# Performance work log

Hardware: AMD Instinct MI355X
Metric: run time of the kernel (lower is better)

Reference implementation:

```python
import jax, jax.numpy as jnp
import numpy as np

N, D_IN, D_BLOCK, D_OUT, E, K = 65536, 128, 256, 128, 8, 2


def setup_inputs() -> dict:
    key = jax.random.key(0)
    ks = jax.random.split(key, 8)
    s_in = 1.0 / np.sqrt(D_IN)
    s_h = 1.0 / np.sqrt(D_BLOCK)
    return {
        "x": jax.random.normal(ks[0], (N, D_IN), jnp.float32),
        "Wg": jax.random.normal(ks[1], (D_IN, E), jnp.float32) * s_in,
        "W1": jax.random.normal(ks[2], (E, D_IN, D_BLOCK), jnp.float32) * s_in,
        "b1": jax.random.normal(ks[3], (E, D_BLOCK), jnp.float32) * 0.01,
        "W2": jax.random.normal(ks[4], (E, D_BLOCK, D_BLOCK), jnp.float32) * s_h,
        "b2": jax.random.normal(ks[5], (E, D_BLOCK), jnp.float32) * 0.01,
        "Wo": jax.random.normal(ks[6], (D_BLOCK, D_OUT), jnp.float32) * s_h,
        "bo": jax.random.normal(ks[7], (D_OUT,), jnp.float32) * 0.01,
    }


def reference(x, Wg, W1, b1, W2, b2, Wo, bo):
    # Router: linear gate -> top-k -> softmax over the k selected logits,
    # scattered back to a dense [N, E] combine-weight matrix (zeros elsewhere).
    logits = x @ Wg                                   # [N, E]
    topv, topi = jax.lax.top_k(logits, K)             # [N, K]
    w_topk = jax.nn.softmax(topv, axis=-1)            # [N, K]
    onehot = jax.nn.one_hot(topi, E, dtype=x.dtype)   # [N, K, E]
    weights = jnp.einsum("nk,nke->ne", w_topk, onehot)  # [N, E]

    # Expert MLPs (n_blocks=2, ReLU, dropout=0 at eval), computed for all
    # experts over all tokens; unselected experts have weight 0, so the
    # weighted combine reproduces the original masked gather/scatter math.
    h = jax.nn.relu(jnp.einsum("nd,edh->enh", x, W1) + b1[:, None, :])   # [E,N,H]
    h = jax.nn.relu(jnp.einsum("enh,ehg->eng", h, W2) + b2[:, None, :])  # [E,N,H]
    y = jnp.einsum("enh,ho->eno", h, Wo) + bo                             # [E,N,O]

    # Weighted scatter-add combine: outs[n] = sum_e weights[n,e] * y[e,n]
    return jnp.einsum("ne,eno->no", weights, y)
```

## Files before the change

kernel.cpp:

```cpp
#include <hip/hip_runtime.h>
#include <math.h>

typedef unsigned short ushort_t;
typedef __attribute__((ext_vector_type(8))) short bf16x8;
typedef __attribute__((ext_vector_type(4))) float f32x4;
typedef __attribute__((ext_vector_type(8))) unsigned short u16x8;

#define N_TOK 65536
#define DIN 128
#define HD 256
#define DOUT 128
#define NEXP 8
#define MT 64
#define MAX_TILES (N_TOK / MT)

__device__ __forceinline__ unsigned short f2bf(float f) {
    union { float f; unsigned int i; } v; v.f = f;
    unsigned int i = v.i;
    return (unsigned short)((i + 0x7FFFu + ((i >> 16) & 1u)) >> 16);
}

__global__ void pack_weights(const float* __restrict__ W1,
                             const float* __restrict__ W2,
                             const float* __restrict__ Wo,
                             ushort_t* __restrict__ wt1f,
                             ushort_t* __restrict__ wt2f,
                             ushort_t* __restrict__ wotf) {
    int id = blockIdx.x * 256 + threadIdx.x;
    const float* src; ushort_t* dst; int Nn, ksteps, c;
    if (id < 32768) {
        int e = id >> 12; c = id & 4095;
        Nn = HD; ksteps = 4; src = W1 + (size_t)e * DIN * HD; dst = wt1f + (size_t)id * 8;
    } else if (id < 98304) {
        int t = id - 32768; int e = t >> 13; c = t & 8191;
        Nn = HD; ksteps = 8; src = W2 + (size_t)e * HD * HD; dst = wt2f + (size_t)t * 8;
    } else {
        int t = id - 98304; c = t;
        Nn = DOUT; ksteps = 8; src = Wo; dst = wotf + (size_t)t * 8;
    }
    int L = c & 63; int kc = c >> 6;
    int kstep = kc % ksteps; int ntile = kc / ksteps;
    int q = L >> 4, m = L & 15;
    int n = ntile * 16 + m; int k0 = kstep * 32 + q * 8;
    u16x8 v;
#pragma unroll
    for (int j = 0; j < 8; j++) v[j] = f2bf(src[(size_t)(k0 + j) * Nn + n]);
    *(u16x8*)dst = v;
}

#define RT_BLOCK 512
#define RT_TPB 64
__global__ __launch_bounds__(RT_BLOCK)
void router_kernel(const float* __restrict__ x,
                   const float* __restrict__ Wg,
                   int* __restrict__ counts,
                   int* __restrict__ list_tok,
                   float* __restrict__ list_w) {
    __shared__ float wgsT[NEXP * 132];
    __shared__ int lcnt[NEXP];
    __shared__ int lbase[NEXP];
    int tid = threadIdx.x;
    if (tid < NEXP) lcnt[tid] = 0;
    for (int i = tid; i < DIN * NEXP; i += RT_BLOCK) {
        int e = i & 7, k = i >> 3;
        wgsT[e * 132 + k] = Wg[i];
    }
    __syncthreads();

    int e = tid & 7;
    int tl = tid >> 3;
    int n = blockIdx.x * RT_TPB + tl;
    const float4* xr = (const float4*)(x + (size_t)n * DIN);
    const float4* wv4 = (const float4*)(wgsT + e * 132);
    float lg = 0.f;
#pragma unroll
    for (int kk = 0; kk < 32; kk++) {
        float4 xv = xr[kk];
        float4 wv = wv4[kk];
        lg += xv.x * wv.x;
        lg += xv.y * wv.y;
        lg += xv.z * wv.z;
        lg += xv.w * wv.w;
    }
    float v0 = lg; int e0 = e;
#pragma unroll
    for (int d = 1; d < 8; d <<= 1) {
        float ov = __shfl_xor(v0, d, 64);
        int oe = __shfl_xor(e0, d, 64);
        if (ov > v0 || (ov == v0 && oe < e0)) { v0 = ov; e0 = oe; }
    }
    float mv = (e == e0) ? -3.0e38f : lg;
    float v1 = mv; int e1 = e;
#pragma unroll
    for (int d = 1; d < 8; d <<= 1) {
        float ov = __shfl_xor(v1, d, 64);
        int oe = __shfl_xor(e1, d, 64);
        if (ov > v1 || (ov == v1 && oe < e1)) { v1 = ov; e1 = oe; }
    }
    float t = expf(v1 - v0);
    float inv = 1.0f / (1.0f + t);
    float w0 = inv, w1 = t * inv;

    bool writer = (e == 0);
    int p0 = 0, p1 = 0;
    if (writer) {
        p0 = atomicAdd(&lcnt[e0], 1);
        p1 = atomicAdd(&lcnt[e1], 1);
    }
    __syncthreads();
    if (tid < NEXP) lbase[tid] = atomicAdd(&counts[tid], lcnt[tid]);
    __syncthreads();
    if (writer) {
        int q0 = lbase[e0] + p0;
        list_tok[e0 * N_TOK + q0] = n;
        list_w[e0 * N_TOK + q0] = w0;
        int q1 = lbase[e1] + p1;
        list_tok[e1 * N_TOK + q1] = n;
        list_w[e1 * N_TOK + q1] = w1;
    }
}

__global__ void init_out(const float* __restrict__ bo, float* __restrict__ out) {
    int gid = blockIdx.x * 256 + threadIdx.x;
    float4 b = ((const float4*)bo)[gid & 31];
    ((float4*)out)[gid] = b;
}

__global__ __launch_bounds__(256, 3)
void expert_kernel(const float* __restrict__ x,
                   const int* __restrict__ counts,
                   const int* __restrict__ list_tok,
                   const float* __restrict__ list_w,
                   const ushort_t* __restrict__ wt1f,
                   const ushort_t* __restrict__ wt2f,
                   const ushort_t* __restrict__ wotf,
                   const float* __restrict__ b1,
                   const float* __restrict__ b2,
                   float* __restrict__ out) {
    int e = blockIdx.x & 7;
    int tile = blockIdx.x >> 3;
    int cnt = counts[e];
    int base = tile * MT;
    if (base >= cnt) return;
    int rows = cnt - base; if (rows > MT) rows = MT;

    __shared__ __align__(16) ushort_t bufA[8192];
    __shared__ __align__(16) ushort_t bufH[16384];
    __shared__ int toks_s[MT];
    __shared__ float wts_s[MT];

    int tid = threadIdx.x;
    int lane = tid & 63;
    int w = tid >> 6;
    int q = lane >> 4;
    int mcol = lane & 15;

    if (tid < MT) {
        int rr = tid < rows ? tid : rows - 1;
        toks_s[tid] = list_tok[(size_t)e * N_TOK + base + rr];
        wts_s[tid] = list_w[(size_t)e * N_TOK + base + rr];
    }
    for (int c = tid; c < 1024; c += 256) {
        int row = c >> 4;
        int kchunk = c & 15;
        int rr = row < rows ? row : rows - 1;
        int tok = list_tok[(size_t)e * N_TOK + base + rr];
        const float4* src = (const float4*)(x + (size_t)tok * DIN + kchunk * 8);
        float4 lo = src[0], hi = src[1];
        u16x8 v;
        v[0] = f2bf(lo.x); v[1] = f2bf(lo.y); v[2] = f2bf(lo.z); v[3] = f2bf(lo.w);
        v[4] = f2bf(hi.x); v[5] = f2bf(hi.y); v[6] = f2bf(hi.z); v[7] = f2bf(hi.w);
        int kstep = kchunk >> 2, qq = kchunk & 3;
        int dchunk = (kstep * 4 + (row >> 4)) * 64 + qq * 16 + (row & 15);
        ((u16x8*)bufA)[dchunk] = v;
    }
    __syncthreads();

    const bf16x8* Albs = (const bf16x8*)bufA;
    const bf16x8* Hlbs = (const bf16x8*)bufH;

    f32x4 acc[4][4];
#pragma unroll
    for (int mt = 0; mt < 4; mt++)
#pragma unroll
        for (int nt = 0; nt < 4; nt++) acc[mt][nt] = (f32x4){0.f, 0.f, 0.f, 0.f};
    const bf16x8* B1 = (const bf16x8*)(wt1f + (size_t)e * 4096 * 8);
#pragma unroll
    for (int kstep = 0; kstep < 4; kstep++) {
        bf16x8 a[4];
#pragma unroll
        for (int mt = 0; mt < 4; mt++) a[mt] = Albs[(kstep * 4 + mt) * 64 + lane];
#pragma unroll
        for (int nt = 0; nt < 4; nt++) {
            bf16x8 b = B1[((w * 4 + nt) * 4 + kstep) * 64 + lane];
#pragma unroll
            for (int mt = 0; mt < 4; mt++)
                acc[mt][nt] = __builtin_amdgcn_mfma_f32_16x16x32_bf16(a[mt], b, acc[mt][nt], 0, 0, 0);
        }
    }
#pragma unroll
    for (int nt = 0; nt < 4; nt++) {
        int nn = (w * 4 + nt) * 16 + mcol;
        float bias = b1[e * HD + nn];
        int kstep = nn >> 5, qq = (nn >> 3) & 3, jj = nn & 7;
#pragma unroll
        for (int mt = 0; mt < 4; mt++) {
#pragma unroll
            for (int r = 0; r < 4; r++) {
                float v = acc[mt][nt][r] + bias;
                v = v > 0.f ? v : 0.f;
                int chunk = (kstep * 4 + mt) * 64 + qq * 16 + q * 4 + r;
                bufH[chunk * 8 + jj] = f2bf(v);
            }
        }
    }
    __syncthreads();

    f32x4 acc2[4][4];
#pragma unroll
    for (int mt = 0; mt < 4; mt++)
#pragma unroll
        for (int nt = 0; nt < 4; nt++) acc2[mt][nt] = (f32x4){0.f, 0.f, 0.f, 0.f};
    const bf16x8* B2 = (const bf16x8*)(wt2f + (size_t)e * 8192 * 8);
#pragma unroll
    for (int kstep = 0; kstep < 8; kstep++) {
        bf16x8 a[4];
#pragma unroll
        for (int mt = 0; mt < 4; mt++) a[mt] = Hlbs[(kstep * 4 + mt) * 64 + lane];
#pragma unroll
        for (int nt = 0; nt < 4; nt++) {
            bf16x8 b = B2[((w * 4 + nt) * 8 + kstep) * 64 + lane];
#pragma unroll
            for (int mt = 0; mt < 4; mt++)
                acc2[mt][nt] = __builtin_amdgcn_mfma_f32_16x16x32_bf16(a[mt], b, acc2[mt][nt], 0, 0, 0);
        }
    }
    __syncthreads();
#pragma unroll
    for (int nt = 0; nt < 4; nt++) {
        int nn = (w * 4 + nt) * 16 + mcol;
        float bias = b2[e * HD + nn];
        int kstep = nn >> 5, qq = (nn >> 3) & 3, jj = nn & 7;
#pragma unroll
        for (int mt = 0; mt < 4; mt++) {
#pragma unroll
            for (int r = 0; r < 4; r++) {
                float v = acc2[mt][nt][r] + bias;
                v = v > 0.f ? v : 0.f;
                int chunk = (kstep * 4 + mt) * 64 + qq * 16 + q * 4 + r;
                bufH[chunk * 8 + jj] = f2bf(v);
            }
        }
    }
    __syncthreads();

    f32x4 acc3[4][2];
#pragma unroll
    for (int mt = 0; mt < 4; mt++)
#pragma unroll
        for (int nt = 0; nt < 2; nt++) acc3[mt][nt] = (f32x4){0.f, 0.f, 0.f, 0.f};
    const bf16x8* B3 = (const bf16x8*)wotf;
#pragma unroll
    for (int kstep = 0; kstep < 8; kstep++) {
        bf16x8 a[4];
#pragma unroll
        for (int mt = 0; mt < 4; mt++) a[mt] = Hlbs[(kstep * 4 + mt) * 64 + lane];
#pragma unroll
        for (int nt = 0; nt < 2; nt++) {
            bf16x8 b = B3[((w * 2 + nt) * 8 + kstep) * 64 + lane];
#pragma unroll
            for (int mt = 0; mt < 4; mt++)
                acc3[mt][nt] = __builtin_amdgcn_mfma_f32_16x16x32_bf16(a[mt], b, acc3[mt][nt], 0, 0, 0);
        }
    }
#pragma unroll
    for (int mt = 0; mt < 4; mt++) {
#pragma unroll
        for (int r = 0; r < 4; r++) {
            int row = mt * 16 + q * 4 + r;
            if (row < rows) {
                int tok = toks_s[row];
                float wgt = wts_s[row];
                float* dst = out + (size_t)tok * DOUT;
#pragma unroll
                for (int nt = 0; nt < 2; nt++) {
                    int col = (w * 2 + nt) * 16 + mcol;
                    atomicAdd(&dst[col], wgt * acc3[mt][nt][r]);
                }
            }
        }
    }
}

extern "C" void kernel_launch(void* const* d_in, const int* in_sizes, int n_in,
                              void* d_out, int out_size, void* d_ws, size_t ws_size,
                              hipStream_t stream) {
    const float* x  = (const float*)d_in[0];
    const float* Wg = (const float*)d_in[1];
    const float* W1 = (const float*)d_in[2];
    const float* b1 = (const float*)d_in[3];
    const float* W2 = (const float*)d_in[4];
    const float* b2 = (const float*)d_in[5];
    const float* Wo = (const float*)d_in[6];
    const float* bo = (const float*)d_in[7];
    float* out = (float*)d_out;

    char* ws = (char*)d_ws;
    size_t off = 0;
    int* counts    = (int*)(ws + off);    off += 256;
    int* list_tok  = (int*)(ws + off);    off += (size_t)NEXP * N_TOK * 4;
    float* list_w  = (float*)(ws + off);  off += (size_t)NEXP * N_TOK * 4;
    ushort_t* wt1f = (ushort_t*)(ws + off); off += (size_t)NEXP * DIN * HD * 2;
    ushort_t* wt2f = (ushort_t*)(ws + off); off += (size_t)NEXP * HD * HD * 2;
    ushort_t* wotf = (ushort_t*)(ws + off); off += (size_t)HD * DOUT * 2;

    hipMemsetAsync(counts, 0, 256, stream);
    pack_weights<<<400, 256, 0, stream>>>(W1, W2, Wo, wt1f, wt2f, wotf);
    router_kernel<<<N_TOK / RT_TPB, RT_BLOCK, 0, stream>>>(x, Wg, counts, list_tok, list_w);
    init_out<<<(N_TOK * DOUT / 4) / 256, 256, 0, stream>>>(bo, out);
    expert_kernel<<<NEXP * MAX_TILES, 256, 0, stream>>>(x, counts, list_tok, list_w,
                                                        wt1f, wt2f, wotf, b1, b2, out);
}
```

Baseline: 199.8 us.

## Fuse packing and output init into router, prefetch weights, use transposed LDS reads

Folds the weight-packing and output-bias initialization kernels into the router kernel, removing two launches. In the expert kernel, weight fragments are double-buffered in registers to prefetch the next k-step, biases are hoisted, and f32->bf16 conversion uses packed v_cvt_pk_bf16_f32. Hidden activations are now stored row-major with vectorized 8-byte writes and read back with ds_read_b64_tr_b16 transposed LDS loads instead of scalar 2-byte scattered stores. This raises register pressure and relies on inline asm with manual waitcnt.

Result: faster. 178.8 us (-10.5%).

```diff
diff --git a/kernel.cpp b/kernel.cpp
--- a/kernel.cpp
+++ b/kernel.cpp
@@ -3,8 +3,11 @@
 
 typedef unsigned short ushort_t;
 typedef __attribute__((ext_vector_type(8))) short bf16x8;
+typedef __attribute__((ext_vector_type(4))) short bf16x4;
 typedef __attribute__((ext_vector_type(4))) float f32x4;
 typedef __attribute__((ext_vector_type(8))) unsigned short u16x8;
+typedef __attribute__((ext_vector_type(2))) unsigned int u32x2;
+typedef __attribute__((ext_vector_type(4))) unsigned int u32x4;
 
 #define N_TOK 65536
 #define DIN 128
@@ -20,50 +23,62 @@
     return (unsigned short)((i + 0x7FFFu + ((i >> 16) & 1u)) >> 16);
 }
 
-__global__ void pack_weights(const float* __restrict__ W1,
-                             const float* __restrict__ W2,
-                             const float* __restrict__ Wo,
-                             ushort_t* __restrict__ wt1f,
-                             ushort_t* __restrict__ wt2f,
-                             ushort_t* __restrict__ wotf) {
-    int id = blockIdx.x * 256 + threadIdx.x;
-    const float* src; ushort_t* dst; int Nn, ksteps, c;
-    if (id < 32768) {
-        int e = id >> 12; c = id & 4095;
-        Nn = HD; ksteps = 4; src = W1 + (size_t)e * DIN * HD; dst = wt1f + (size_t)id * 8;
-    } else if (id < 98304) {
-        int t = id - 32768; int e = t >> 13; c = t & 8191;
-        Nn = HD; ksteps = 8; src = W2 + (size_t)e * HD * HD; dst = wt2f + (size_t)t * 8;
-    } else {
-        int t = id - 98304; c = t;
-        Nn = DOUT; ksteps = 8; src = Wo; dst = wotf + (size_t)t * 8;
-    }
-    int L = c & 63; int kc = c >> 6;
-    int kstep = kc % ksteps; int ntile = kc / ksteps;
-    int q = L >> 4, m = L & 15;
-    int n = ntile * 16 + m; int k0 = kstep * 32 + q * 8;
-    u16x8 v;
-#pragma unroll
-    for (int j = 0; j < 8; j++) v[j] = f2bf(src[(size_t)(k0 + j) * Nn + n]);
-    *(u16x8*)dst = v;
-}
-
 #define RT_BLOCK 512
 #define RT_TPB 64
+
 __global__ __launch_bounds__(RT_BLOCK)
 void router_kernel(const float* __restrict__ x,
                    const float* __restrict__ Wg,
+                   const float* __restrict__ W1,
+                   const float* __restrict__ W2,
+                   const float* __restrict__ Wo,
+                   const float* __restrict__ bo,
                    int* __restrict__ counts,
                    int* __restrict__ list_tok,
-                   float* __restrict__ list_w) {
+                   float* __restrict__ list_w,
+                   ushort_t* __restrict__ wt1f,
+                   ushort_t* __restrict__ wt2f,
+                   ushort_t* __restrict__ wotf,
+                   float* __restrict__ out) {
     __shared__ float wgsT[NEXP * 132];
     __shared__ int lcnt[NEXP];
     __shared__ int lbase[NEXP];
     int tid = threadIdx.x;
     if (tid < NEXP) lcnt[tid] = 0;
     for (int i = tid; i < DIN * NEXP; i += RT_BLOCK) {
-        int e = i & 7, k = i >> 3;
-        wgsT[e * 132 + k] = Wg[i];
+        int ee = i & 7, k = i >> 3;
+        wgsT[ee * 132 + k] = Wg[i];
+    }
+    {
+        const float4* bo4 = (const float4*)bo;
+        float4* ob = (float4*)(out + (size_t)blockIdx.x * RT_TPB * DOUT);
+#pragma unroll
+        for (int i = 0; i < 4; i++) {
+            int idx = i * RT_BLOCK + tid;
+            ob[idx] = bo4[idx & 31];
+        }
+    }
+    if (blockIdx.x < 200) {
+        int id = blockIdx.x * RT_BLOCK + tid;
+        const float* src; ushort_t* dst; int Nn, ksteps, c;
+        if (id < 32768) {
+            int ee = id >> 12; c = id & 4095;
+            Nn = HD; ksteps = 4; src = W1 + (size_t)ee * DIN * HD; dst = wt1f + (size_t)id * 8;
+        } else if (id < 98304) {
+            int t = id - 32768; int ee = t >> 13; c = t & 8191;
+            Nn = HD; ksteps = 8; src = W2 + (size_t)ee * HD * HD; dst = wt2f + (size_t)t * 8;
+        } else {
+            int t = id - 98304; c = t;
+            Nn = DOUT; ksteps = 8; src = Wo; dst = wotf + (size_t)t * 8;
+        }
+        int L = c & 63; int kc = c >> 6;
+        int kstep = kc % ksteps; int ntile = kc / ksteps;
+        int qq = L >> 4, mm = L & 15;
+        int n = ntile * 16 + mm; int k0 = kstep * 32 + qq * 8;
+        u16x8 v;
+#pragma unroll
+        for (int j = 0; j < 8; j++) v[j] = f2bf(src[(size_t)(k0 + j) * Nn + n]);
+        *(u16x8*)dst = v;
     }
     __syncthreads();
 
@@ -118,12 +133,6 @@
         list_tok[e1 * N_TOK + q1] = n;
         list_w[e1 * N_TOK + q1] = w1;
     }
-}
-
-__global__ void init_out(const float* __restrict__ bo, float* __restrict__ out) {
-    int gid = blockIdx.x * 256 + threadIdx.x;
-    float4 b = ((const float4*)bo)[gid & 31];
-    ((float4*)out)[gid] = b;
 }
 
 __global__ __launch_bounds__(256, 3)
@@ -160,6 +169,19 @@
         toks_s[tid] = list_tok[(size_t)e * N_TOK + base + rr];
         wts_s[tid] = list_w[(size_t)e * N_TOK + base + rr];
     }
+
+    float bias1[4], bias2[4];
+#pragma unroll
+    for (int nt = 0; nt < 4; nt++) {
+        int nn = (w * 4 + nt) * 16 + mcol;
+        bias1[nt] = b1[e * HD + nn];
+        bias2[nt] = b2[e * HD + nn];
+    }
+    const bf16x8* B1 = (const bf16x8*)(wt1f + (size_t)e * 4096 * 8);
+    bf16x8 b1r[2][4];
+#pragma unroll
+    for (int nt = 0; nt < 4; nt++) b1r[0][nt] = B1[((w * 4 + nt) * 4 + 0) * 64 + lane];
+
     for (int c = tid; c < 1024; c += 256) {
         int row = c >> 4;
         int kchunk = c & 15;
@@ -167,89 +189,120 @@
         int tok = list_tok[(size_t)e * N_TOK + base + rr];
         const float4* src = (const float4*)(x + (size_t)tok * DIN + kchunk * 8);
         float4 lo = src[0], hi = src[1];
-        u16x8 v;
-        v[0] = f2bf(lo.x); v[1] = f2bf(lo.y); v[2] = f2bf(lo.z); v[3] = f2bf(lo.w);
-        v[4] = f2bf(hi.x); v[5] = f2bf(hi.y); v[6] = f2bf(hi.z); v[7] = f2bf(hi.w);
+        unsigned p0, p1, p2, p3;
+        asm("v_cvt_pk_bf16_f32 %0, %1, %2" : "=v"(p0) : "v"(lo.x), "v"(lo.y));
+        asm("v_cvt_pk_bf16_f32 %0, %1, %2" : "=v"(p1) : "v"(lo.z), "v"(lo.w));
+        asm("v_cvt_pk_bf16_f32 %0, %1, %2" : "=v"(p2) : "v"(hi.x), "v"(hi.y));
+        asm("v_cvt_pk_bf16_f32 %0, %1, %2" : "=v"(p3) : "v"(hi.z), "v"(hi.w));
         int kstep = kchunk >> 2, qq = kchunk & 3;
         int dchunk = (kstep * 4 + (row >> 4)) * 64 + qq * 16 + (row & 15);
-        ((u16x8*)bufA)[dchunk] = v;
+        u32x4 v; v.x = p0; v.y = p1; v.z = p2; v.w = p3;
+        *(u32x4*)(&bufA[dchunk * 8]) = v;
     }
     __syncthreads();
 
     const bf16x8* Albs = (const bf16x8*)bufA;
-    const bf16x8* Hlbs = (const bf16x8*)bufH;
 
     f32x4 acc[4][4];
 #pragma unroll
     for (int mt = 0; mt < 4; mt++)
 #pragma unroll
         for (int nt = 0; nt < 4; nt++) acc[mt][nt] = (f32x4){0.f, 0.f, 0.f, 0.f};
-    const bf16x8* B1 = (const bf16x8*)(wt1f + (size_t)e * 4096 * 8);
 #pragma unroll
     for (int kstep = 0; kstep < 4; kstep++) {
+        const int cur = kstep & 1, nxt = cur ^ 1;
+        if (kstep < 3) {
+#pragma unroll
+            for (int nt = 0; nt < 4; nt++)
+                b1r[nxt][nt] = B1[((w * 4 + nt) * 4 + kstep + 1) * 64 + lane];
+        }
         bf16x8 a[4];
 #pragma unroll
         for (int mt = 0; mt < 4; mt++) a[mt] = Albs[(kstep * 4 + mt) * 64 + lane];
 #pragma unroll
-        for (int nt = 0; nt < 4; nt++) {
-            bf16x8 b = B1[((w * 4 + nt) * 4 + kstep) * 64 + lane];
+        for (int nt = 0; nt < 4; nt++)
 #pragma unroll
             for (int mt = 0; mt < 4; mt++)
-                acc[mt][nt] = __builtin_amdgcn_mfma_f32_16x16x32_bf16(a[mt], b, acc[mt][nt], 0, 0, 0);
-        }
-    }
+                acc[mt][nt] = __builtin_amdgcn_mfma_f32_16x16x32_bf16(a[mt], b1r[cur][nt], acc[mt][nt], 0, 0, 0);
+    }
+
+    const bf16x8* B2 = (const bf16x8*)(wt2f + (size_t)e * 8192 * 8);
+    bf16x8 b2r[2][4];
+#pragma unroll
+    for (int nt = 0; nt < 4; nt++) b2r[0][nt] = B2[((w * 4 + nt) * 8 + 0) * 64 + lane];
+
 #pragma unroll
     for (int nt = 0; nt < 4; nt++) {
-        int nn = (w * 4 + nt) * 16 + mcol;
-        float bias = b1[e * HD + nn];
-        int kstep = nn >> 5, qq = (nn >> 3) & 3, jj = nn & 7;
+        int off0 = w * 2048 + nt * 512 + (mcol >> 2) * 128 + (mcol & 3) * 32 + q * 8;
 #pragma unroll
         for (int mt = 0; mt < 4; mt++) {
-#pragma unroll
-            for (int r = 0; r < 4; r++) {
-                float v = acc[mt][nt][r] + bias;
-                v = v > 0.f ? v : 0.f;
-                int chunk = (kstep * 4 + mt) * 64 + qq * 16 + q * 4 + r;
-                bufH[chunk * 8 + jj] = f2bf(v);
-            }
-        }
-    }
-    __syncthreads();
+            float v0 = acc[mt][nt][0] + bias1[nt]; v0 = v0 > 0.f ? v0 : 0.f;
+            float v1 = acc[mt][nt][1] + bias1[nt]; v1 = v1 > 0.f ? v1 : 0.f;
+            float v2 = acc[mt][nt][2] + bias1[nt]; v2 = v2 > 0.f ? v2 : 0.f;
+            float v3 = acc[mt][nt][3] + bias1[nt]; v3 = v3 > 0.f ? v3 : 0.f;
+            unsigned d0, d1;
+            asm("v_cvt_pk_bf16_f32 %0, %1, %2" : "=v"(d0) : "v"(v0), "v"(v1));
+            asm("v_cvt_pk_bf16_f32 %0, %1, %2" : "=v"(d1) : "v"(v2), "v"(v3));
+            u32x2 dd; dd.x = d0; dd.y = d1;
+            *(u32x2*)(&bufH[(mt * 8192 + off0) >> 1]) = dd;
+        }
+    }
+    __syncthreads();
+
+    unsigned trb = ((unsigned)(size_t)(void*)bufH) + (unsigned)(q * 256 + mcol * 8);
 
     f32x4 acc2[4][4];
 #pragma unroll
     for (int mt = 0; mt < 4; mt++)
 #pragma unroll
         for (int nt = 0; nt < 4; nt++) acc2[mt][nt] = (f32x4){0.f, 0.f, 0.f, 0.f};
-    const bf16x8* B2 = (const bf16x8*)(wt2f + (size_t)e * 8192 * 8);
 #pragma unroll
     for (int kstep = 0; kstep < 8; kstep++) {
+        const int cur = kstep & 1, nxt = cur ^ 1;
+        if (kstep < 7) {
+#pragma unroll
+            for (int nt = 0; nt < 4; nt++)
+                b2r[nxt][nt] = B2[((w * 4 + nt) * 8 + kstep + 1) * 64 + lane];
+        }
         bf16x8 a[4];
 #pragma unroll
-        for (int mt = 0; mt < 4; mt++) a[mt] = Hlbs[(kstep * 4 + mt) * 64 + lane];
-#pragma unroll
-        for (int nt = 0; nt < 4; nt++) {
-            bf16x8 b = B2[((w * 4 + nt) * 8 + kstep) * 64 + lane];
+        for (int mt = 0; mt < 4; mt++) {
+            bf16x4 lo, hi;
+            unsigned ad = trb + (unsigned)(mt * 8192 + kstep * 1024);
+            asm volatile("ds_read_b64_tr_b16 %0, %2\n\t"
+                         "ds_read_b64_tr_b16 %1, %2 offset:128"
+                         : "=&v"(lo), "=&v"(hi) : "v"(ad));
+            a[mt] = __builtin_shufflevector(lo, hi, 0, 1, 2, 3, 4, 5, 6, 7);
+        }
+        asm volatile("s_waitcnt lgkmcnt(0)" ::: "memory");
+        __builtin_amdgcn_sched_barrier(0);
+#pragma unroll
+        for (int nt = 0; nt < 4; nt++)
 #pragma unroll
             for (int mt = 0; mt < 4; mt++)
-                acc2[mt][nt] = __builtin_amdgcn_mfma_f32_16x16x32_bf16(a[mt], b, acc2[mt][nt], 0, 0, 0);
-        }
-    }
-    __syncthreads();
+                acc2[mt][nt] = __builtin_amdgcn_mfma_f32_16x16x32_bf16(a[mt], b2r[cur][nt], acc2[mt][nt], 0, 0, 0);
+    }
+    __syncthreads();
+
+    const bf16x8* B3 = (const bf16x8*)wotf;
+    bf16x8 b3r[2][2];
+#pragma unroll
+    for (int nt = 0; nt < 2; nt++) b3r[0][nt] = B3[((w * 2 + nt) * 8 + 0) * 64 + lane];
+
 #pragma unroll
     for (int nt = 0; nt < 4; nt++) {
-        int nn = (w * 4 + nt) * 16 + mcol;
-        float bias = b2[e * HD + nn];
-        int kstep = nn >> 5, qq = (nn >> 3) & 3, jj = nn & 7;
+        int off0 = w * 2048 + nt * 512 + (mcol >> 2) * 128 + (mcol & 3) * 32 + q * 8;
 #pragma unroll
         for (int mt = 0; mt < 4; mt++) {
-#pragma unroll
-            for (int r = 0; r < 4; r++) {
-                float v = acc2[mt][nt][r] + bias;
-                v = v > 0.f ? v : 0.f;
-                int chunk = (kstep * 4 + mt) * 64 + qq * 16 + q * 4 + r;
-                bufH[chunk * 8 + jj] = f2bf(v);
-            }
+            float v0 = acc2[mt][nt][0] + bias2[nt]; v0 = v0 > 0.f ? v0 : 0.f;
+            float v1 = acc2[mt][nt][1] + bias2[nt]; v1 = v1 > 0.f ? v1 : 0.f;
+            float v2 = acc2[mt][nt][2] + bias2[nt]; v2 = v2 > 0.f ? v2 : 0.f;
+            float v3 = acc2[mt][nt][3] + bias2[nt]; v3 = v3 > 0.f ? v3 : 0.f;
+            unsigned d0, d1;
+            asm("v_cvt_pk_bf16_f32 %0, %1, %2" : "=v"(d0) : "v"(v0), "v"(v1));
+            asm("v_cvt_pk_bf16_f32 %0, %1, %2" : "=v"(d1) : "v"(v2), "v"(v3));
+            u32x2 dd; dd.x = d0; dd.y = d1;
+            *(u32x2*)(&bufH[(mt * 8192 + off0) >> 1]) = dd;
         }
     }
     __syncthreads();
@@ -259,19 +312,31 @@
     for (int mt = 0; mt < 4; mt++)
 #pragma unroll
         for (int nt = 0; nt < 2; nt++) acc3[mt][nt] = (f32x4){0.f, 0.f, 0.f, 0.f};
-    const bf16x8* B3 = (const bf16x8*)wotf;
 #pragma unroll
     for (int kstep = 0; kstep < 8; kstep++) {
+        const int cur = kstep & 1, nxt = cur ^ 1;
+        if (kstep < 7) {
+#pragma unroll
+            for (int nt = 0; nt < 2; nt++)
+                b3r[nxt][nt] = B3[((w * 2 + nt) * 8 + kstep + 1) * 64 + lane];
+        }
         bf16x8 a[4];
 #pragma unroll
-        for (int mt = 0; mt < 4; mt++) a[mt] = Hlbs[(kstep * 4 + mt) * 64 + lane];
-#pragma unroll
-        for (int nt = 0; nt < 2; nt++) {
-            bf16x8 b = B3[((w * 2 + nt) * 8 + kstep) * 64 + lane];
+        for (int mt = 0; mt < 4; mt++) {
+            bf16x4 lo, hi;
+            unsigned ad = trb + (unsigned)(mt * 8192 + kstep * 1024);
+            asm volatile("ds_read_b64_tr_b16 %0, %2\n\t"
+                         "ds_read_b64_tr_b16 %1, %2 offset:128"
+                         : "=&v"(lo), "=&v"(hi) : "v"(ad));
+            a[mt] = __builtin_shufflevector(lo, hi, 0, 1, 2, 3, 4, 5, 6, 7);
+        }
+        asm volatile("s_waitcnt lgkmcnt(0)" ::: "memory");
+        __builtin_amdgcn_sched_barrier(0);
+#pragma unroll
+        for (int nt = 0; nt < 2; nt++)
 #pragma unroll
             for (int mt = 0; mt < 4; mt++)
-                acc3[mt][nt] = __builtin_amdgcn_mfma_f32_16x16x32_bf16(a[mt], b, acc3[mt][nt], 0, 0, 0);
-        }
+                acc3[mt][nt] = __builtin_amdgcn_mfma_f32_16x16x32_bf16(a[mt], b3r[cur][nt], acc3[mt][nt], 0, 0, 0);
     }
 #pragma unroll
     for (int mt = 0; mt < 4; mt++) {
@@ -315,9 +380,8 @@
     ushort_t* wotf = (ushort_t*)(ws + off); off += (size_t)HD * DOUT * 2;
 
     hipMemsetAsync(counts, 0, 256, stream);
-    pack_weights<<<400, 256, 0, stream>>>(W1, W2, Wo, wt1f, wt2f, wotf);
-    router_kernel<<<N_TOK / RT_TPB, RT_BLOCK, 0, stream>>>(x, Wg, counts, list_tok, list_w);
-    init_out<<<(N_TOK * DOUT / 4) / 256, 256, 0, stream>>>(bo, out);
+    router_kernel<<<N_TOK / RT_TPB, RT_BLOCK, 0, stream>>>(
+        x, Wg, W1, W2, Wo, bo, counts, list_tok, list_w, wt1f, wt2f, wotf, out);
     expert_kernel<<<NEXP * MAX_TILES, 256, 0, stream>>>(x, counts, list_tok, list_w,
                                                         wt1f, wt2f, wotf, b1, b2, out);
 }
```
